# Kernel optimization log

Measured on AMD Instinct MI355X. Metric: run time of the kernel, lower is better.

The kernel has to match this reference:

```python
import jax, jax.numpy as jnp
import numpy as np

B, T, D, H = 2, 2048, 2048, 16
HD = D // H  # head dim = 128


def setup_inputs() -> dict:
    key = jax.random.key(0)
    k_x, k_qkv, k_out, k_doc = jax.random.split(key, 4)
    x = jax.random.normal(k_x, (B, T, D), dtype=jnp.float32)
    # real RoPE tables (sin/cos of position * inv_freq), shape (T, HD)
    inv_freq = 1.0 / (10000.0 ** (jnp.arange(0, HD, 2, dtype=jnp.float32) / HD))
    ang = jnp.arange(T, dtype=jnp.float32)[:, None] * inv_freq[None, :]  # (T, HD/2)
    ang = jnp.concatenate([ang, ang], axis=-1)  # (T, HD)
    sin, cos = jnp.sin(ang), jnp.cos(ang)
    W_qkv = jax.random.normal(k_qkv, (D, 3 * D), dtype=jnp.float32) * 0.02
    W_out = jax.random.normal(k_out, (D, D), dtype=jnp.float32) * 0.02
    # sorted doc ids per row -> contiguous packed documents
    doc_ids = jnp.sort(jax.random.randint(k_doc, (B, T), 0, 8), axis=-1).astype(jnp.int32)
    return {"x": x, "sin": sin, "cos": cos, "W_qkv": W_qkv, "W_out": W_out, "doc_ids": doc_ids}


def _apply_rope(xh, sin, cos):
    # xh: (B, T, H, HD); sin/cos: (T, HD) broadcast over batch & heads
    s = sin[None, :, None, :]
    c = cos[None, :, None, :]
    x1, x2 = jnp.split(xh, 2, axis=-1)
    rot = jnp.concatenate([-x2, x1], axis=-1)  # rotate_half
    return xh * c + rot * s


def reference(x, sin, cos, W_qkv, W_out, doc_ids):
    b, t, d = x.shape
    qkv = x @ W_qkv  # (B, T, 3D), fused QKV projection, no bias
    q, k, v = jnp.split(qkv, 3, axis=-1)
    q = q.reshape(b, t, H, HD)
    k = k.reshape(b, t, H, HD)
    v = v.reshape(b, t, H, HD)
    q = _apply_rope(q, sin, cos)
    k = _apply_rope(k, sin, cos)
    # doc-causal additive bias: (B, 1, T, T)
    neg_inf = jnp.finfo(q.dtype).min / 2
    causal = jnp.tril(jnp.ones((t, t), dtype=jnp.bool_))
    same_doc = doc_ids[:, :, None] == doc_ids[:, None, :]
    mask = (causal[None, :, :] & same_doc)[:, None, :, :]
    bias = jnp.where(mask, 0.0, neg_inf).astype(q.dtype)
    # attention (matches jax.nn.dot_product_attention with additive bias)
    scale = 1.0 / jnp.sqrt(jnp.asarray(HD, dtype=q.dtype))
    scores = jnp.einsum("bqhd,bkhd->bhqk", q, k) * scale + bias
    attn = jax.nn.softmax(scores, axis=-1)
    out = jnp.einsum("bhqk,bkhd->bqhd", attn, v)  # (B, T, H, HD)
    out = out.reshape(b, t, d)
    return out @ W_out
```

## Files before the change

kernel.cpp:

```cpp
#include <hip/hip_runtime.h>
#include <hip/hip_bf16.h>

#define BB 2
#define TT 2048
#define DD 2048
#define HH 16
#define HDIM 128
#define BT 4096
#define N3 6144

typedef __attribute__((ext_vector_type(8))) short s16x8;
typedef __attribute__((ext_vector_type(4))) float f32x4;

static __device__ __forceinline__ ushort f2bf(float x) {
  union { float f; unsigned u; } cv; cv.f = x;
  unsigned r = cv.u + 0x7FFF + ((cv.u >> 16) & 1);
  return (ushort)(r >> 16);
}
static __device__ __forceinline__ float bf2f(ushort u) {
  union { unsigned u; float f; } cv; cv.u = ((unsigned)u) << 16; return cv.f;
}

#define GLDS16(gp, lp) __builtin_amdgcn_global_load_lds( \
    (const __attribute__((address_space(1))) void*)(gp), \
    (__attribute__((address_space(3))) void*)(lp), 16, 0, 0)

__global__ void cvt_kernel(const float* __restrict__ in, ushort* __restrict__ out, int n4) {
  int i = blockIdx.x * blockDim.x + threadIdx.x;
  if (i < n4) {
    float4 v = ((const float4*)in)[i];
    ushort4 o;
    o.x = f2bf(v.x); o.y = f2bf(v.y); o.z = f2bf(v.z); o.w = f2bf(v.w);
    ((ushort4*)out)[i] = o;
  }
}

__global__ void transpose_cvt(const float* __restrict__ in, ushort* __restrict__ out, int R, int C) {
  __shared__ float tile[32][33];
  const int bx = blockIdx.x * 32, by = blockIdx.y * 32;
  const int tx = threadIdx.x, ty = threadIdx.y;
  #pragma unroll
  for (int i = 0; i < 32; i += 8)
    tile[ty + i][tx] = in[(size_t)(by + ty + i) * C + bx + tx];
  __syncthreads();
  #pragma unroll
  for (int i = 0; i < 32; i += 8)
    out[(size_t)(bx + ty + i) * R + by + tx] = f2bf(tile[tx][ty + i]);
}

__global__ __launch_bounds__(512, 1)
void gemm8_qkv(const ushort* __restrict__ A, const ushort* __restrict__ Bt,
               ushort* __restrict__ Qb, ushort* __restrict__ Kb, ushort* __restrict__ Vb)
{
  constexpr int K = 2048;
  constexpr int NT = K / 64;
  __shared__ char smem[131072];

  const int tid = threadIdx.x, wave = tid >> 6, lane = tid & 63;
  const int lr = lane & 15, lg = lane >> 4;
  const int wm = wave >> 2, wn = wave & 3;

  const int wg = blockIdx.x;
  const int xcd = wg & 7, l = wg >> 3;
  const int rgrp = xcd >> 2, cgrp = xcd & 3;
  const int lrow = l & 7, lcol = l >> 3;
  const int by = rgrp * 8 + lrow, bx = cgrp * 6 + lcol;
  const int m0 = by * 256, n0 = bx * 256;

  auto stage2 = [&](const ushort* src, int base0, int U, char* region) {
    #pragma unroll
    for (int inst = 0; inst < 4; ++inst) {
      const int c = inst * 512 + tid;
      const int row = c >> 3;
      const int colb = (c & 7) * 16;
      const int colsw = colb ^ (((row >> 2) & 1) << 5);
      const ushort* gp = src + (size_t)(base0 + row) * K + U * 64 + (colsw >> 1);
      GLDS16(gp, region + inst * 8192 + wave * 1024);
    }
  };

  f32x4 acc[8][4] = {};

  stage2(A,  m0, 0, smem);
  stage2(Bt, n0, 0, smem + 32768);
  stage2(A,  m0, 1, smem + 65536);
  asm volatile("s_waitcnt vmcnt(4)" ::: "memory");
  __builtin_amdgcn_s_barrier();

  for (int T = 0; T < NT; ++T) {
    const int buf = T & 1;
    char* Ab = smem + (buf << 16);
    char* Bb = smem + (buf << 16) + 32768;
    s16x8 a[8];
    #pragma unroll
    for (int p = 0; p < 4; ++p) {
      const int kk = p >> 1, qn = p & 1;
      if ((p & 1) == 0) {
        #pragma unroll
        for (int mf = 0; mf < 8; ++mf) {
          const int r = wm * 128 + mf * 16 + lr;
          a[mf] = *(const s16x8*)(Ab + r * 128 + ((kk * 64 + lg * 16) ^ (((r >> 2) & 1) << 5)));
        }
      }
      s16x8 b[2];
      #pragma unroll
      for (int nf = 0; nf < 2; ++nf) {
        const int r = wn * 64 + (qn * 2 + nf) * 16 + lr;
        b[nf] = *(const s16x8*)(Bb + r * 128 + ((kk * 64 + lg * 16) ^ (((r >> 2) & 1) << 5)));
      }
      if (p == 0 && T + 1 < NT) stage2(Bt, n0, T + 1, smem + (((T + 1) & 1) << 16) + 32768);
      if (p == 3 && T + 2 < NT) stage2(A,  m0, T + 2, smem + ((buf) << 16));
      __builtin_amdgcn_s_barrier();
      asm volatile("s_waitcnt lgkmcnt(0)" ::: "memory");
      __builtin_amdgcn_sched_barrier(0);
      __builtin_amdgcn_s_setprio(1);
      #pragma unroll
      for (int mf = 0; mf < 8; ++mf)
        #pragma unroll
        for (int nf = 0; nf < 2; ++nf)
          acc[mf][qn * 2 + nf] =
            __builtin_amdgcn_mfma_f32_16x16x32_bf16(a[mf], b[nf], acc[mf][qn * 2 + nf], 0, 0, 0);
      __builtin_amdgcn_s_setprio(0);
      if (p == 3) {
        if (T < NT - 2) { asm volatile("s_waitcnt vmcnt(4)" ::: "memory"); }
        else            { asm volatile("s_waitcnt vmcnt(0)" ::: "memory"); }
      }
      __builtin_amdgcn_s_barrier();
    }
  }

  #pragma unroll
  for (int mf = 0; mf < 8; ++mf) {
    #pragma unroll
    for (int nn = 0; nn < 4; ++nn) {
      #pragma unroll
      for (int r = 0; r < 4; ++r) {
        const int rowg = m0 + wm * 128 + mf * 16 + lg * 4 + r;
        const int colg = n0 + wn * 64 + nn * 16 + lr;
        const int which = colg >> 11, rem = colg & 2047;
        const int hh = rem >> 7, d = rem & 127;
        const int b2 = rowg >> 11, t = rowg & 2047;
        ushort* dstp = (which == 0) ? Qb : (which == 1) ? Kb : Vb;
        dstp[(((size_t)b2 * HH + hh) * TT + t) * HDIM + d] = f2bf(acc[mf][nn][r]);
      }
    }
  }
}

__global__ __launch_bounds__(256, 2)
void gemm_bt2(const ushort* __restrict__ A, const ushort* __restrict__ Bt,
              float* __restrict__ Cf, int M, int N, int K)
{
  __shared__ ushort As[128 * 32];
  __shared__ ushort Bs[128 * 32];
  const int tid = threadIdx.x;
  const int wave = tid >> 6, lane = tid & 63;
  const int lr = lane & 15, lg = lane >> 4;
  const int m0 = blockIdx.y * 128, n0 = blockIdx.x * 128;
  const int wm = (wave & 1) * 64, wn = (wave >> 1) * 64;
  f32x4 acc[4][4] = {};

  for (int k0 = 0; k0 < K; k0 += 32) {
    __syncthreads();
    #pragma unroll
    for (int call = 0; call < 2; ++call) {
      const int base = call * 256 + wave * 64;
      const int c = base + lane;
      const int row = c >> 2, cc = c & 3;
      GLDS16(A  + (size_t)(m0 + row) * K + k0 + cc * 8, As + (size_t)base * 8);
      GLDS16(Bt + (size_t)(n0 + row) * K + k0 + cc * 8, Bs + (size_t)base * 8);
    }
    __syncthreads();
    s16x8 a[4], b[4];
    #pragma unroll
    for (int i = 0; i < 4; ++i) a[i] = *(const s16x8*)&As[(wm + i * 16 + lr) * 32 + lg * 8];
    #pragma unroll
    for (int i = 0; i < 4; ++i) b[i] = *(const s16x8*)&Bs[(wn + i * 16 + lr) * 32 + lg * 8];
    #pragma unroll
    for (int mi = 0; mi < 4; ++mi)
      #pragma unroll
      for (int ni = 0; ni < 4; ++ni)
        acc[mi][ni] = __builtin_amdgcn_mfma_f32_16x16x32_bf16(a[mi], b[ni], acc[mi][ni], 0, 0, 0);
  }

  #pragma unroll
  for (int mi = 0; mi < 4; ++mi)
    #pragma unroll
    for (int ni = 0; ni < 4; ++ni)
      #pragma unroll
      for (int r = 0; r < 4; ++r) {
        const int row = m0 + wm + mi * 16 + lg * 4 + r;
        const int col = n0 + wn + ni * 16 + lr;
        Cf[(size_t)row * N + col] = acc[mi][ni][r];
      }
}

__global__ void rope_inplace(ushort* __restrict__ Qb, ushort* __restrict__ Kb,
                             const float* __restrict__ sinp, const float* __restrict__ cosp) {
  const int idx = blockIdx.x * 256 + threadIdx.x;
  const int d = idx & 63;
  const int t = (idx >> 6) & (TT - 1);
  const int bh = idx >> 17;
  const float c = cosp[t * HDIM + d];
  const float s = sinp[t * HDIM + d];
  const size_t base = ((size_t)bh * TT + t) * HDIM + d;
  float q1 = bf2f(Qb[base]), q2 = bf2f(Qb[base + 64]);
  Qb[base]      = f2bf(q1 * c - q2 * s);
  Qb[base + 64] = f2bf(q2 * c + q1 * s);
  float k1 = bf2f(Kb[base]), k2 = bf2f(Kb[base + 64]);
  Kb[base]      = f2bf(k1 * c - k2 * s);
  Kb[base + 64] = f2bf(k2 * c + k1 * s);
}

__global__ __launch_bounds__(256, 2)
void attn_kernel(const ushort* __restrict__ Qb, const ushort* __restrict__ Kb,
                 const ushort* __restrict__ Vb, const int* __restrict__ doc,
                 ushort* __restrict__ Ob)
{
  __shared__ ushort Ks[64 * 128];
  __shared__ ushort VTs[128 * 64];
  __shared__ ushort Ps[4][16 * 64];
  const int qt = blockIdx.x, h = blockIdx.y, b = blockIdx.z;
  const int q0 = qt * 64;
  const int tid = threadIdx.x, wave = tid >> 6, lane = tid & 63;
  const int lr = lane & 15, lg = lane >> 4;
  const size_t bh = (size_t)b * HH + h;
  const int* docb = doc + b * TT;

  const ushort* Qp = Qb + (bh * TT + q0 + wave * 16) * HDIM;
  s16x8 aq[4];
  #pragma unroll
  for (int ks = 0; ks < 4; ++ks) aq[ks] = *(const s16x8*)&Qp[lr * HDIM + ks * 32 + lg * 8];

  int qdoc[4];
  #pragma unroll
  for (int r = 0; r < 4; ++r) qdoc[r] = docb[q0 + wave * 16 + lg * 4 + r];
  const int qdoc0 = docb[q0];

  float m2[4], lsum[4];
  #pragma unroll
  for (int r = 0; r < 4; ++r) { m2[r] = -1e30f; lsum[r] = 0.f; }
  f32x4 oacc[8] = {};

  const float sc = 0.08838834764831843f * 1.4426950408889634f;

  const ushort* Kbase = Kb + bh * TT * HDIM;
  const ushort* Vbase = Vb + bh * TT * HDIM;

  const int ntiles = qt + 1;
  for (int kt = 0; kt < ntiles; ++kt) {
    const int kv0 = kt * 64;
    if (docb[kv0 + 63] < qdoc0) continue;
    __syncthreads();
    #pragma unroll
    for (int i = 0; i < 4; ++i) {
      const int c = tid + i * 256;
      const int row = c >> 4, c8 = c & 15;
      s16x8 v = *(const s16x8*)&Kbase[(size_t)(kv0 + row) * HDIM + c8 * 8];
      const int off = (row * 256 + c8 * 16) ^ ((row & 7) << 4);
      *(s16x8*)((char*)Ks + off) = v;
    }
    #pragma unroll
    for (int i = 0; i < 4; ++i) {
      const int c = tid + i * 256;
      const int kv = c >> 4, d8 = c & 15;
      s16x8 v = *(const s16x8*)&Vbase[(size_t)(kv0 + kv) * HDIM + d8 * 8];
      #pragma unroll
      for (int j = 0; j < 8; ++j) {
        const int d = d8 * 8 + j;
        const int off = (d * 128 + kv * 2) ^ ((d & 7) << 4);
        *(ushort*)((char*)VTs + off) = (ushort)v[j];
      }
    }
    __syncthreads();

    f32x4 sfrag[4] = {};
    #pragma unroll
    for (int ks = 0; ks < 4; ++ks) {
      #pragma unroll
      for (int ct = 0; ct < 4; ++ct) {
        const int row = ct * 16 + lr;
        const int off = (row * 256 + ks * 64 + lg * 16) ^ ((row & 7) << 4);
        s16x8 bk = *(const s16x8*)((char*)Ks + off);
        sfrag[ct] = __builtin_amdgcn_mfma_f32_16x16x32_bf16(aq[ks], bk, sfrag[ct], 0, 0, 0);
      }
    }

    int kd[4];
    #pragma unroll
    for (int ct = 0; ct < 4; ++ct) kd[ct] = docb[kv0 + ct * 16 + lr];

    float s[4][4], tmax[4];
    #pragma unroll
    for (int r = 0; r < 4; ++r) tmax[r] = -1e30f;
    #pragma unroll
    for (int ct = 0; ct < 4; ++ct) {
      const int col = kv0 + ct * 16 + lr;
      #pragma unroll
      for (int r = 0; r < 4; ++r) {
        const int row = q0 + wave * 16 + lg * 4 + r;
        float v = sfrag[ct][r] * sc;
        const bool keep = (col <= row) && (kd[ct] == qdoc[r]);
        v = keep ? v : -1e30f;
        s[ct][r] = v;
        tmax[r] = fmaxf(tmax[r], v);
      }
    }
    #pragma unroll
    for (int r = 0; r < 4; ++r) {
      #pragma unroll
      for (int off = 8; off >= 1; off >>= 1)
        tmax[r] = fmaxf(tmax[r], __shfl_xor(tmax[r], off, 16));
    }
    float alpha[4];
    #pragma unroll
    for (int r = 0; r < 4; ++r) {
      const float mnew = fmaxf(m2[r], tmax[r]);
      alpha[r] = exp2f(m2[r] - mnew);
      m2[r] = mnew;
      lsum[r] *= alpha[r];
    }
    #pragma unroll
    for (int ct = 0; ct < 4; ++ct) {
      #pragma unroll
      for (int r = 0; r < 4; ++r) {
        const float p = (s[ct][r] > -1e29f) ? exp2f(s[ct][r] - m2[r]) : 0.f;
        lsum[r] += p;
        const int prow = lg * 4 + r;
        const int off = (prow * 128 + (ct * 16 + lr) * 2) ^ ((prow & 7) << 4);
        *(ushort*)((char*)&Ps[wave][0] + off) = f2bf(p);
      }
    }
    #pragma unroll
    for (int oc = 0; oc < 8; ++oc)
      #pragma unroll
      for (int r = 0; r < 4; ++r) oacc[oc][r] *= alpha[r];
    #pragma unroll
    for (int ks = 0; ks < 2; ++ks) {
      const int poff = (lr * 128 + ks * 64 + lg * 16) ^ ((lr & 7) << 4);
      s16x8 ap = *(const s16x8*)((char*)&Ps[wave][0] + poff);
      #pragma unroll
      for (int oc = 0; oc < 8; ++oc) {
        const int vrow = oc * 16 + lr;
        const int voff = (vrow * 128 + ks * 64 + lg * 16) ^ ((vrow & 7) << 4);
        s16x8 bv = *(const s16x8*)((char*)VTs + voff);
        oacc[oc] = __builtin_amdgcn_mfma_f32_16x16x32_bf16(ap, bv, oacc[oc], 0, 0, 0);
      }
    }
  }

  #pragma unroll
  for (int r = 0; r < 4; ++r)
    #pragma unroll
    for (int off = 8; off >= 1; off >>= 1)
      lsum[r] += __shfl_xor(lsum[r], off, 16);

  ushort* Op = Ob + ((size_t)b * TT + q0 + wave * 16) * DD + (size_t)h * HDIM;
  #pragma unroll
  for (int oc = 0; oc < 8; ++oc)
    #pragma unroll
    for (int r = 0; r < 4; ++r)
      Op[(lg * 4 + r) * DD + oc * 16 + lr] = f2bf(oacc[oc][r] / lsum[r]);
}

extern "C" void kernel_launch(void* const* d_in, const int* in_sizes, int n_in,
                              void* d_out, int out_size, void* d_ws, size_t ws_size,
                              hipStream_t stream)
{
  const float* x    = (const float*)d_in[0];
  const float* sinp = (const float*)d_in[1];
  const float* cosp = (const float*)d_in[2];
  const float* Wqkv = (const float*)d_in[3];
  const float* Wout = (const float*)d_in[4];
  const int*   doc  = (const int*)d_in[5];
  float* out = (float*)d_out;

  ushort* xb  = (ushort*)d_ws;
  ushort* WqT = xb  + (size_t)BT * DD;
  ushort* WoT = WqT + (size_t)N3 * DD;
  ushort* Qb  = WoT + (size_t)DD * DD;
  ushort* Kb  = Qb  + (size_t)BB * TT * DD;
  ushort* Vb  = Kb  + (size_t)BB * TT * DD;
  ushort* Ob  = Vb  + (size_t)BB * TT * DD;

  cvt_kernel<<<(BT * DD / 4 + 255) / 256, 256, 0, stream>>>(x, xb, BT * DD / 4);
  transpose_cvt<<<dim3(N3 / 32, DD / 32), dim3(32, 8), 0, stream>>>(Wqkv, WqT, DD, N3);
  transpose_cvt<<<dim3(DD / 32, DD / 32), dim3(32, 8), 0, stream>>>(Wout, WoT, DD, DD);
  gemm8_qkv<<<dim3((N3 / 256) * (BT / 256)), 512, 0, stream>>>(xb, WqT, Qb, Kb, Vb);
  rope_inplace<<<BB * HH * TT * 64 / 256, 256, 0, stream>>>(Qb, Kb, sinp, cosp);
  attn_kernel<<<dim3(TT / 64, HH, BB), 256, 0, stream>>>(Qb, Kb, Vb, doc, Ob);
  gemm_bt2<<<dim3(DD / 128, BT / 128), 256, 0, stream>>>(Ob, WoT, out, BT, DD, DD);
}
```

Before: 407.6 us.

## Simplify QKV GEMM pipeline to whole-tile double buffering with one barrier

Replaces the four-phase, split A/B staggered prefetch schedule in the QKV GEMM with a plain double buffer. The whole next K-tile is prefetched at the start of each iteration, both k-substeps run with all A and B fragments loaded up front, and a single wait plus barrier closes each tile. LDS fragment offsets are precomputed once outside the loop. This removes many per-phase barriers and cuts address arithmetic, but it gives up the finer interleaving of global loads with MFMA work. Each tile now ends with a full vmcnt(0) wait, which can expose memory latency.

```diff
diff --git a/kernel.cpp b/kernel.cpp
--- a/kernel.cpp
+++ b/kernel.cpp
@@ -67,66 +67,67 @@
   const int by = rgrp * 8 + lrow, bx = cgrp * 6 + lcol;
   const int m0 = by * 256, n0 = bx * 256;
 
-  auto stage2 = [&](const ushort* src, int base0, int U, char* region) {
+  int offA[8], offB[4];
+  #pragma unroll
+  for (int mf = 0; mf < 8; ++mf) {
+    const int r = wm * 128 + mf * 16 + lr;
+    offA[mf] = r * 128 + ((lg * 16) ^ (((r >> 2) & 1) << 5));
+  }
+  #pragma unroll
+  for (int nf = 0; nf < 4; ++nf) {
+    const int r = wn * 64 + nf * 16 + lr;
+    offB[nf] = r * 128 + ((lg * 16) ^ (((r >> 2) & 1) << 5));
+  }
+
+  auto stage = [&](int U, int bufsel) {
+    char* baseA = smem + (bufsel << 16);
+    char* baseB = baseA + 32768;
     #pragma unroll
     for (int inst = 0; inst < 4; ++inst) {
       const int c = inst * 512 + tid;
       const int row = c >> 3;
       const int colb = (c & 7) * 16;
       const int colsw = colb ^ (((row >> 2) & 1) << 5);
-      const ushort* gp = src + (size_t)(base0 + row) * K + U * 64 + (colsw >> 1);
-      GLDS16(gp, region + inst * 8192 + wave * 1024);
+      GLDS16(A  + (size_t)(m0 + row) * K + U * 64 + (colsw >> 1), baseA + inst * 8192 + wave * 1024);
+    }
+    #pragma unroll
+    for (int inst = 0; inst < 4; ++inst) {
+      const int c = inst * 512 + tid;
+      const int row = c >> 3;
+      const int colb = (c & 7) * 16;
+      const int colsw = colb ^ (((row >> 2) & 1) << 5);
+      GLDS16(Bt + (size_t)(n0 + row) * K + U * 64 + (colsw >> 1), baseB + inst * 8192 + wave * 1024);
     }
   };
 
   f32x4 acc[8][4] = {};
 
-  stage2(A,  m0, 0, smem);
-  stage2(Bt, n0, 0, smem + 32768);
-  stage2(A,  m0, 1, smem + 65536);
-  asm volatile("s_waitcnt vmcnt(4)" ::: "memory");
+  stage(0, 0);
+  asm volatile("s_waitcnt vmcnt(0)" ::: "memory");
   __builtin_amdgcn_s_barrier();
 
   for (int T = 0; T < NT; ++T) {
     const int buf = T & 1;
-    char* Ab = smem + (buf << 16);
-    char* Bb = smem + (buf << 16) + 32768;
-    s16x8 a[8];
-    #pragma unroll
-    for (int p = 0; p < 4; ++p) {
-      const int kk = p >> 1, qn = p & 1;
-      if ((p & 1) == 0) {
-        #pragma unroll
-        for (int mf = 0; mf < 8; ++mf) {
-          const int r = wm * 128 + mf * 16 + lr;
-          a[mf] = *(const s16x8*)(Ab + r * 128 + ((kk * 64 + lg * 16) ^ (((r >> 2) & 1) << 5)));
-        }
-      }
-      s16x8 b[2];
-      #pragma unroll
-      for (int nf = 0; nf < 2; ++nf) {
-        const int r = wn * 64 + (qn * 2 + nf) * 16 + lr;
-        b[nf] = *(const s16x8*)(Bb + r * 128 + ((kk * 64 + lg * 16) ^ (((r >> 2) & 1) << 5)));
-      }
-      if (p == 0 && T + 1 < NT) stage2(Bt, n0, T + 1, smem + (((T + 1) & 1) << 16) + 32768);
-      if (p == 3 && T + 2 < NT) stage2(A,  m0, T + 2, smem + ((buf) << 16));
-      __builtin_amdgcn_s_barrier();
-      asm volatile("s_waitcnt lgkmcnt(0)" ::: "memory");
-      __builtin_amdgcn_sched_barrier(0);
+    if (T + 1 < NT) stage(T + 1, buf ^ 1);
+    const char* Ab = smem + (buf << 16);
+    const char* Bb = Ab + 32768;
+    #pragma unroll
+    for (int kk = 0; kk < 2; ++kk) {
+      s16x8 af[8], bf[4];
+      #pragma unroll
+      for (int mf = 0; mf < 8; ++mf) af[mf] = *(const s16x8*)(Ab + kk * 64 + offA[mf]);
+      #pragma unroll
+      for (int nf = 0; nf < 4; ++nf) bf[nf] = *(const s16x8*)(Bb + kk * 64 + offB[nf]);
       __builtin_amdgcn_s_setprio(1);
       #pragma unroll
       for (int mf = 0; mf < 8; ++mf)
         #pragma unroll
-        for (int nf = 0; nf < 2; ++nf)
-          acc[mf][qn * 2 + nf] =
-            __builtin_amdgcn_mfma_f32_16x16x32_bf16(a[mf], b[nf], acc[mf][qn * 2 + nf], 0, 0, 0);
+        for (int nf = 0; nf < 4; ++nf)
+          acc[mf][nf] = __builtin_amdgcn_mfma_f32_16x16x32_bf16(af[mf], bf[nf], acc[mf][nf], 0, 0, 0);
       __builtin_amdgcn_s_setprio(0);
-      if (p == 3) {
-        if (T < NT - 2) { asm volatile("s_waitcnt vmcnt(4)" ::: "memory"); }
-        else            { asm volatile("s_waitcnt vmcnt(0)" ::: "memory"); }
-      }
-      __builtin_amdgcn_s_barrier();
-    }
+    }
+    asm volatile("s_waitcnt vmcnt(0) lgkmcnt(0)" ::: "memory");
+    __builtin_amdgcn_s_barrier();
   }
 
   #pragma unroll
```

Result: faster. 393.6 us (-3.5%).
